# Performance work log

Hardware: AMD Instinct MI355X
Metric: run time of the kernel (lower is better)

## Reference

```python
import jax, jax.numpy as jnp
import numpy as np

N_NODES = 50000
N_EDGES = 800000


def _gcn_conv(x, W, b, src, dst, deg_inv_sqrt, n_nodes):
    # PyG GCNConv: h = x @ W, then symmetric-normalized sum aggregation
    h = x @ W  # [N, F_out]
    norm = deg_inv_sqrt[src] * deg_inv_sqrt[dst]  # [E_aug]
    msg = h[src] * norm[:, None]  # [E_aug, F_out]
    out = jax.ops.segment_sum(msg, dst, num_segments=n_nodes)
    return out + b


def setup_inputs() -> dict:
    key = jax.random.key(0)
    k1, k2, k3, k4 = jax.random.split(key, 4)
    x = jax.random.normal(k1, (N_NODES, 128), dtype=jnp.float32)
    edge_index = jax.random.randint(k2, (2, N_EDGES), 0, N_NODES, dtype=jnp.int64)
    W1 = jax.random.normal(k3, (128, 64), dtype=jnp.float32) * (1.0 / np.sqrt(128))
    b1 = jnp.zeros((64,), dtype=jnp.float32)
    W2 = jax.random.normal(k4, (64, 32), dtype=jnp.float32) * (1.0 / np.sqrt(64))
    b2 = jnp.zeros((32,), dtype=jnp.float32)
    return {"x": x, "edge_index": edge_index, "W1": W1, "b1": b1, "W2": W2, "b2": b2}


def reference(x, edge_index, W1, b1, W2, b2):
    n_nodes = x.shape[0]
    # add self-loops (PyG GCNConv default)
    loop = jnp.arange(n_nodes, dtype=edge_index.dtype)
    src = jnp.concatenate([edge_index[0], loop])
    dst = jnp.concatenate([edge_index[1], loop])
    # symmetric normalization: deg from target index (gcn_norm)
    deg = jax.ops.segment_sum(jnp.ones_like(dst, dtype=x.dtype), dst, num_segments=n_nodes)
    deg_inv_sqrt = jnp.where(deg > 0, jax.lax.rsqrt(jnp.maximum(deg, 1.0)), 0.0)

    h = _gcn_conv(x, W1, b1, src, dst, deg_inv_sqrt, n_nodes)
    h = jax.nn.relu(h)
    # dropout is identity in eval mode (reference runs inference)
    out = _gcn_conv(h, W2, b2, src, dst, deg_inv_sqrt, n_nodes)
    return out
```

## Files before the change

### kernel.cpp

```cpp
#include <hip/hip_runtime.h>
#include <hip/hip_fp16.h>


#define F_IN 128
#define F_MID 64
#define F_OUT 32
#define NBLK 512
#define CAP 8192
#define CAPN 64

#define RFL(x) __builtin_amdgcn_readfirstlane(x)

__device__ __forceinline__ void h8acc(float* a, const uint4& v) {
    const __half2* hp = (const __half2*)&v;
#pragma unroll
    for (int i = 0; i < 4; ++i) {
        float2 f = __half22float2(hp[i]);
        a[2 * i]     += f.x;
        a[2 * i + 1] += f.y;
    }
}

__device__ __forceinline__ void h8unpack(float* f, const uint4& v) {
    const __half2* hp = (const __half2*)&v;
#pragma unroll
    for (int i = 0; i < 4; ++i) {
        float2 t = __half22float2(hp[i]);
        f[2 * i]     = t.x;
        f[2 * i + 1] = t.y;
    }
}

__device__ __forceinline__ uint4 pack8(const float4& a, const float4& b) {
    union { uint4 u; __half2 h[4]; } pk;
    pk.h[0] = __float22half2_rn(make_float2(a.x, a.y));
    pk.h[1] = __float22half2_rn(make_float2(a.z, a.w));
    pk.h[2] = __float22half2_rn(make_float2(b.x, b.y));
    pk.h[3] = __float22half2_rn(make_float2(b.z, b.w));
    return pk.u;
}

__global__ __launch_bounds__(256) void k_build_scatter(
    const int* __restrict__ src, const int* __restrict__ dst, int E, int chunk,
    int nbuk, int* __restrict__ cursor, int* __restrict__ esort) {
    __shared__ int cnt[256];
    __shared__ int off[256];
    int t = threadIdx.x;
    cnt[t] = 0;
    __syncthreads();
    int e0 = blockIdx.x * chunk;
    int e1 = min(E, e0 + chunk);
    for (int e = e0 + t; e < e1; e += 256)
        atomicAdd(&cnt[dst[e] >> 8], 1);
    __syncthreads();
    if (t < nbuk) {
        int c = cnt[t];
        off[t] = t * CAP + (c ? atomicAdd(&cursor[t], c) : 0);
    }
    __syncthreads();
    for (int e = e0 + t; e < e1; e += 256) {
        int d = dst[e];
        int pos = atomicAdd(&off[d >> 8], 1);
        esort[pos] = (src[e] << 8) | (d & 255);
    }
}

__global__ __launch_bounds__(256) void k_bucket_pad(
    const int* __restrict__ esort, const int* __restrict__ cursor, int n,
    int* __restrict__ deg, int* __restrict__ elist) {
    __shared__ int cur[256];
    int b = blockIdx.x;
    int t = threadIdx.x;
    int node0 = b << 8;
    int e0 = b * CAP;
    int e1 = e0 + min(cursor[b], CAP);
    cur[t] = 0;
    __syncthreads();
    for (int e = e0 + t; e < e1; e += 256) {
        int p = esort[e];
        int local = p & 255;
        int pos = atomicAdd(&cur[local], 1);
        if (pos < CAPN)
            elist[((node0 + local) << 6) + pos] = p >> 8;
    }
    __syncthreads();
    int node = node0 + t;
    if (node < n) deg[node] = cur[t];
}

__global__ __launch_bounds__(256, 4) void k_gemm1(
    const float* __restrict__ x, const float* __restrict__ W1,
    const int* __restrict__ deg, uint4* __restrict__ g1h, int n) {
    __shared__ float xs[64 * 129];
    int tid  = threadIdx.x;
    int row0 = blockIdx.x * 64;
    for (int i = tid; i < 64 * (F_IN / 4); i += 256) {
        int r = i >> 5, k4 = i & 31;
        int gr = row0 + r;
        float4 v = make_float4(0.f, 0.f, 0.f, 0.f);
        if (gr < n) v = ((const float4*)x)[(size_t)gr * 32 + k4];
        float* p = &xs[r * 129 + k4 * 4];
        p[0] = v.x; p[1] = v.y; p[2] = v.z; p[3] = v.w;
    }
    __syncthreads();
    int w = RFL(tid >> 6);
    int r = tid & 63;
    const float4* W4 = (const float4*)W1;
    float4 a0 = {0.f,0.f,0.f,0.f}, a1 = a0, a2 = a0, a3 = a0;
#pragma unroll 4
    for (int k = 0; k < F_IN; ++k) {
        float xv = xs[r * 129 + k];
        float4 w0 = W4[k * 16 + w * 4 + 0];
        float4 w1 = W4[k * 16 + w * 4 + 1];
        float4 w2 = W4[k * 16 + w * 4 + 2];
        float4 w3 = W4[k * 16 + w * 4 + 3];
        a0.x += xv * w0.x; a0.y += xv * w0.y; a0.z += xv * w0.z; a0.w += xv * w0.w;
        a1.x += xv * w1.x; a1.y += xv * w1.y; a1.z += xv * w1.z; a1.w += xv * w1.w;
        a2.x += xv * w2.x; a2.y += xv * w2.y; a2.z += xv * w2.z; a2.w += xv * w2.w;
        a3.x += xv * w3.x; a3.y += xv * w3.y; a3.z += xv * w3.z; a3.w += xv * w3.w;
    }
    int gr = row0 + r;
    if (gr < n) {
        float dv = rsqrtf((float)(deg[gr] + 1));
        a0.x *= dv; a0.y *= dv; a0.z *= dv; a0.w *= dv;
        a1.x *= dv; a1.y *= dv; a1.z *= dv; a1.w *= dv;
        a2.x *= dv; a2.y *= dv; a2.z *= dv; a2.w *= dv;
        a3.x *= dv; a3.y *= dv; a3.z *= dv; a3.w *= dv;
        g1h[(size_t)gr * 8 + w * 2 + 0] = pack8(a0, a1);
        g1h[(size_t)gr * 8 + w * 2 + 1] = pack8(a2, a3);
    }
}

__global__ __launch_bounds__(256) void k_gather1(
    const int* __restrict__ deg, const int* __restrict__ elist,
    const uint4* __restrict__ g1h, const float* __restrict__ b1,
    uint4* __restrict__ h16, int n) {
    int wave = RFL(threadIdx.x >> 6);
    int lane = threadIdx.x & 63;
    int q    = lane & 7;
    int slot = lane >> 3;
    int d    = blockIdx.x * 4 + wave;
    if (d >= n) return;
    int rawdeg = RFL(deg[d]);
    int cnt  = min(rawdeg, CAPN);
    int base = d << 6;
    float a[8] = {0,0,0,0,0,0,0,0};
    float b[8] = {0,0,0,0,0,0,0,0};
    if (slot == 0) {
        uint4 v = g1h[(size_t)d * 8 + q];
        h8acc(a, v);
    }
    int j = 0;
    for (; j + 32 <= cnt; j += 32) {
        int s0 = elist[base + j + slot];
        int s1 = elist[base + j + 8 + slot];
        int s2 = elist[base + j + 16 + slot];
        int s3 = elist[base + j + 24 + slot];
        uint4 v0 = g1h[(size_t)s0 * 8 + q];
        uint4 v1 = g1h[(size_t)s1 * 8 + q];
        uint4 v2 = g1h[(size_t)s2 * 8 + q];
        uint4 v3 = g1h[(size_t)s3 * 8 + q];
        h8acc(a, v0); h8acc(b, v1); h8acc(a, v2); h8acc(b, v3);
    }
    for (; j + 16 <= cnt; j += 16) {
        int s0 = elist[base + j + slot];
        int s1 = elist[base + j + 8 + slot];
        uint4 v0 = g1h[(size_t)s0 * 8 + q];
        uint4 v1 = g1h[(size_t)s1 * 8 + q];
        h8acc(a, v0); h8acc(b, v1);
    }
    for (; j + 8 <= cnt; j += 8) {
        int s = elist[base + j + slot];
        uint4 v = g1h[(size_t)s * 8 + q];
        h8acc(a, v);
    }
    if (slot < cnt - j) {
        int s = elist[base + j + slot];
        uint4 v = g1h[(size_t)s * 8 + q];
        h8acc(a, v);
    }
#pragma unroll
    for (int i = 0; i < 8; ++i) a[i] += b[i];
#pragma unroll
    for (int i = 0; i < 8; ++i) a[i] += __shfl_xor(a[i], 8);
#pragma unroll
    for (int i = 0; i < 8; ++i) a[i] += __shfl_xor(a[i], 16);
#pragma unroll
    for (int i = 0; i < 8; ++i) a[i] += __shfl_xor(a[i], 32);
    if (slot == 0) {
        float dv = rsqrtf((float)(rawdeg + 1));
        float4 bv0 = ((const float4*)b1)[q * 2 + 0];
        float4 bv1 = ((const float4*)b1)[q * 2 + 1];
        float4 o0, o1;
        o0.x = fmaxf(a[0] * dv + bv0.x, 0.f);
        o0.y = fmaxf(a[1] * dv + bv0.y, 0.f);
        o0.z = fmaxf(a[2] * dv + bv0.z, 0.f);
        o0.w = fmaxf(a[3] * dv + bv0.w, 0.f);
        o1.x = fmaxf(a[4] * dv + bv1.x, 0.f);
        o1.y = fmaxf(a[5] * dv + bv1.y, 0.f);
        o1.z = fmaxf(a[6] * dv + bv1.z, 0.f);
        o1.w = fmaxf(a[7] * dv + bv1.w, 0.f);
        h16[(size_t)d * 8 + q] = pack8(o0, o1);
    }
}

__global__ __launch_bounds__(256, 4) void k_gemm2(
    const uint4* __restrict__ h16, const float* __restrict__ W2,
    const int* __restrict__ deg, uint4* __restrict__ g2h, int n) {
    __shared__ float hs[64 * 65];
    int tid  = threadIdx.x;
    int row0 = blockIdx.x * 64;
    for (int i = tid; i < 64 * 8; i += 256) {
        int r = i >> 3, q = i & 7;
        int gr = row0 + r;
        float f[8] = {0,0,0,0,0,0,0,0};
        if (gr < n) {
            uint4 v = h16[(size_t)gr * 8 + q];
            h8unpack(f, v);
        }
        float* p = &hs[r * 65 + q * 8];
#pragma unroll
        for (int k = 0; k < 8; ++k) p[k] = f[k];
    }
    __syncthreads();
    int w = RFL(tid >> 6);
    int r = tid & 63;
    const float4* W4 = (const float4*)W2;
    float4 a0 = {0.f,0.f,0.f,0.f}, a1 = a0;
#pragma unroll 4
    for (int k = 0; k < F_MID; ++k) {
        float hv = hs[r * 65 + k];
        float4 w0 = W4[k * 8 + w * 2 + 0];
        float4 w1 = W4[k * 8 + w * 2 + 1];
        a0.x += hv * w0.x; a0.y += hv * w0.y; a0.z += hv * w0.z; a0.w += hv * w0.w;
        a1.x += hv * w1.x; a1.y += hv * w1.y; a1.z += hv * w1.z; a1.w += hv * w1.w;
    }
    int gr = row0 + r;
    if (gr < n) {
        float dv = rsqrtf((float)(deg[gr] + 1));
        a0.x *= dv; a0.y *= dv; a0.z *= dv; a0.w *= dv;
        a1.x *= dv; a1.y *= dv; a1.z *= dv; a1.w *= dv;
        g2h[(size_t)gr * 4 + w] = pack8(a0, a1);
    }
}

__global__ __launch_bounds__(256) void k_gather2(
    const int* __restrict__ deg, const int* __restrict__ elist,
    const uint4* __restrict__ g2h, const float* __restrict__ b2,
    float* __restrict__ out, int n) {
    int wave = RFL(threadIdx.x >> 6);
    int lane = threadIdx.x & 63;
    int q    = lane & 3;
    int slot = lane >> 2;
    int d    = blockIdx.x * 4 + wave;
    if (d >= n) return;
    int rawdeg = RFL(deg[d]);
    int cnt  = min(rawdeg, CAPN);
    int base = d << 6;
    float a[8] = {0,0,0,0,0,0,0,0};
    float b[8] = {0,0,0,0,0,0,0,0};
    if (slot == 0) {
        uint4 v = g2h[(size_t)d * 4 + q];
        h8acc(a, v);
    }
    int j = 0;
    for (; j + 64 <= cnt; j += 64) {
        int s0 = elist[base + j + slot];
        int s1 = elist[base + j + 16 + slot];
        int s2 = elist[base + j + 32 + slot];
        int s3 = elist[base + j + 48 + slot];
        uint4 v0 = g2h[(size_t)s0 * 4 + q];
        uint4 v1 = g2h[(size_t)s1 * 4 + q];
        uint4 v2 = g2h[(size_t)s2 * 4 + q];
        uint4 v3 = g2h[(size_t)s3 * 4 + q];
        h8acc(a, v0); h8acc(b, v1); h8acc(a, v2); h8acc(b, v3);
    }
    for (; j + 32 <= cnt; j += 32) {
        int s0 = elist[base + j + slot];
        int s1 = elist[base + j + 16 + slot];
        uint4 v0 = g2h[(size_t)s0 * 4 + q];
        uint4 v1 = g2h[(size_t)s1 * 4 + q];
        h8acc(a, v0); h8acc(b, v1);
    }
    for (; j + 16 <= cnt; j += 16) {
        int s = elist[base + j + slot];
        uint4 v = g2h[(size_t)s * 4 + q];
        h8acc(a, v);
    }
    if (slot < cnt - j) {
        int s = elist[base + j + slot];
        uint4 v = g2h[(size_t)s * 4 + q];
        h8acc(a, v);
    }
#pragma unroll
    for (int i = 0; i < 8; ++i) a[i] += b[i];
#pragma unroll
    for (int i = 0; i < 8; ++i) a[i] += __shfl_xor(a[i], 4);
#pragma unroll
    for (int i = 0; i < 8; ++i) a[i] += __shfl_xor(a[i], 8);
#pragma unroll
    for (int i = 0; i < 8; ++i) a[i] += __shfl_xor(a[i], 16);
#pragma unroll
    for (int i = 0; i < 8; ++i) a[i] += __shfl_xor(a[i], 32);
    if (slot == 0) {
        float dv = rsqrtf((float)(rawdeg + 1));
        float4 bv0 = ((const float4*)b2)[q * 2 + 0];
        float4 bv1 = ((const float4*)b2)[q * 2 + 1];
        float4 o0, o1;
        o0.x = a[0] * dv + bv0.x;
        o0.y = a[1] * dv + bv0.y;
        o0.z = a[2] * dv + bv0.z;
        o0.w = a[3] * dv + bv0.w;
        o1.x = a[4] * dv + bv1.x;
        o1.y = a[5] * dv + bv1.y;
        o1.z = a[6] * dv + bv1.z;
        o1.w = a[7] * dv + bv1.w;
        float4* O4 = (float4*)out;
        O4[(size_t)d * 8 + q * 2 + 0] = o0;
        O4[(size_t)d * 8 + q * 2 + 1] = o1;
    }
}

extern "C" void kernel_launch(void* const* d_in, const int* in_sizes, int n_in,
                              void* d_out, int out_size, void* d_ws, size_t ws_size,
                              hipStream_t stream) {
    const float* x  = (const float*)d_in[0];
    const int*   ei = (const int*)d_in[1];
    const float* W1 = (const float*)d_in[2];
    const float* b1 = (const float*)d_in[3];
    const float* W2 = (const float*)d_in[4];
    const float* b2 = (const float*)d_in[5];

    int n = in_sizes[0] / F_IN;
    int E = in_sizes[1] / 2;
    const int* src = ei;
    const int* dst = ei + E;

    int nbuk  = (n + 255) >> 8;
    int chunk = (E + NBLK - 1) / NBLK;

    char* ws = (char*)d_ws;
    size_t off = 0;
    auto alloc = [&](size_t bytes) {
        char* p = ws + off;
        off += (bytes + 255) & ~(size_t)255;
        return p;
    };
    int*   cursor = (int*)  alloc((size_t)nbuk * 4);
    int*   esort  = (int*)  alloc((size_t)nbuk * CAP * 4);
    int*   deg    = (int*)  alloc((size_t)n * 4);
    int*   elist  = (int*)  alloc((size_t)n * CAPN * 4);
    uint4* g1h    = (uint4*)alloc((size_t)n * F_MID * 2);
    uint4* h16    = (uint4*)alloc((size_t)n * F_MID * 2);
    uint4* g2h    = (uint4*)alloc((size_t)n * F_OUT * 2);

    hipMemsetAsync(cursor, 0, (size_t)nbuk * 4, stream);
    k_build_scatter<<<NBLK, 256, 0, stream>>>(src, dst, E, chunk, nbuk, cursor, esort);
    k_bucket_pad<<<nbuk, 256, 0, stream>>>(esort, cursor, n, deg, elist);

    k_gemm1<<<(n + 63) / 64, 256, 0, stream>>>(x, W1, deg, g1h, n);
    k_gather1<<<(n + 3) / 4, 256, 0, stream>>>(deg, elist, g1h, b1, h16, n);
    k_gemm2<<<(n + 63) / 64, 256, 0, stream>>>(h16, W2, deg, g2h, n);
    k_gather2<<<(n + 3) / 4, 256, 0, stream>>>(deg, elist, g2h, b2,
                                               (float*)d_out, n);
}
```

Baseline: 173.5 us.

## Merge edge scatter with gemm1 and move degree scaling into bucket pad

The edge bucketing scatter and the first dense GEMM now run as one launch, with separate block ranges handling each, so the GEMM no longer waits on the degree computation. The GEMM writes unscaled fp32 output, and the bucket-pad kernel applies the rsqrt degree scaling and fp16 packing once degrees are known. The fp32 intermediate is aliased with the later h16/g2h buffers. This removes one launch and lets the scatter and GEMM overlap, but adds an extra fp32 write and read of the n×64 intermediate.

Result: no change. 171.0 us (-1.5%).

```diff
diff --git a/kernel.cpp b/kernel.cpp
--- a/kernel.cpp
+++ b/kernel.cpp
@@ -40,34 +40,73 @@
     return pk.u;
 }
 
-__global__ __launch_bounds__(256) void k_build_scatter(
+__global__ __launch_bounds__(256, 4) void k_build_gemm1(
     const int* __restrict__ src, const int* __restrict__ dst, int E, int chunk,
-    int nbuk, int* __restrict__ cursor, int* __restrict__ esort) {
-    __shared__ int cnt[256];
-    __shared__ int off[256];
+    int nbuk, int* __restrict__ cursor, int* __restrict__ esort,
+    const float* __restrict__ x, const float* __restrict__ W1,
+    float* __restrict__ g1raw, int n) {
+    __shared__ float xs[64 * 129];
     int t = threadIdx.x;
-    cnt[t] = 0;
+    if (blockIdx.x < NBLK) {
+        int* cnt = (int*)xs;
+        int* off = ((int*)xs) + 256;
+        cnt[t] = 0;
+        __syncthreads();
+        int e0 = blockIdx.x * chunk;
+        int e1 = min(E, e0 + chunk);
+        for (int e = e0 + t; e < e1; e += 256)
+            atomicAdd(&cnt[dst[e] >> 8], 1);
+        __syncthreads();
+        if (t < nbuk) {
+            int c = cnt[t];
+            off[t] = t * CAP + (c ? atomicAdd(&cursor[t], c) : 0);
+        }
+        __syncthreads();
+        for (int e = e0 + t; e < e1; e += 256) {
+            int d = dst[e];
+            int pos = atomicAdd(&off[d >> 8], 1);
+            esort[pos] = (src[e] << 8) | (d & 255);
+        }
+        return;
+    }
+    int row0 = (blockIdx.x - NBLK) * 64;
+    for (int i = t; i < 64 * (F_IN / 4); i += 256) {
+        int r = i >> 5, k4 = i & 31;
+        int gr = row0 + r;
+        float4 v = make_float4(0.f, 0.f, 0.f, 0.f);
+        if (gr < n) v = ((const float4*)x)[(size_t)gr * 32 + k4];
+        float* p = &xs[r * 129 + k4 * 4];
+        p[0] = v.x; p[1] = v.y; p[2] = v.z; p[3] = v.w;
+    }
     __syncthreads();
-    int e0 = blockIdx.x * chunk;
-    int e1 = min(E, e0 + chunk);
-    for (int e = e0 + t; e < e1; e += 256)
-        atomicAdd(&cnt[dst[e] >> 8], 1);
-    __syncthreads();
-    if (t < nbuk) {
-        int c = cnt[t];
-        off[t] = t * CAP + (c ? atomicAdd(&cursor[t], c) : 0);
-    }
-    __syncthreads();
-    for (int e = e0 + t; e < e1; e += 256) {
-        int d = dst[e];
-        int pos = atomicAdd(&off[d >> 8], 1);
-        esort[pos] = (src[e] << 8) | (d & 255);
-    }
-}
-
-__global__ __launch_bounds__(256) void k_bucket_pad(
+    int w = RFL(t >> 6);
+    int r = t & 63;
+    const float4* W4 = (const float4*)W1;
+    float4 a0 = {0.f,0.f,0.f,0.f}, a1 = a0, a2 = a0, a3 = a0;
+#pragma unroll 4
+    for (int k = 0; k < F_IN; ++k) {
+        float xv = xs[r * 129 + k];
+        float4 w0 = W4[k * 16 + w * 4 + 0];
+        float4 w1 = W4[k * 16 + w * 4 + 1];
+        float4 w2 = W4[k * 16 + w * 4 + 2];
+        float4 w3 = W4[k * 16 + w * 4 + 3];
+        a0.x += xv * w0.x; a0.y += xv * w0.y; a0.z += xv * w0.z; a0.w += xv * w0.w;
+        a1.x += xv * w1.x; a1.y += xv * w1.y; a1.z += xv * w1.z; a1.w += xv * w1.w;
+        a2.x += xv * w2.x; a2.y += xv * w2.y; a2.z += xv * w2.z; a2.w += xv * w2.w;
+        a3.x += xv * w3.x; a3.y += xv * w3.y; a3.z += xv * w3.z; a3.w += xv * w3.w;
+    }
+    int gr = row0 + r;
+    if (gr < n) {
+        float4* G = (float4*)g1raw;
+        size_t base = (size_t)gr * 16 + w * 4;
+        G[base + 0] = a0; G[base + 1] = a1; G[base + 2] = a2; G[base + 3] = a3;
+    }
+}
+
+__global__ __launch_bounds__(256) void k_bucket_pad_scale(
     const int* __restrict__ esort, const int* __restrict__ cursor, int n,
-    int* __restrict__ deg, int* __restrict__ elist) {
+    int* __restrict__ deg, int* __restrict__ elist,
+    const float* __restrict__ g1raw, uint4* __restrict__ g1h) {
     __shared__ int cur[256];
     int b = blockIdx.x;
     int t = threadIdx.x;
@@ -86,48 +125,17 @@
     __syncthreads();
     int node = node0 + t;
     if (node < n) deg[node] = cur[t];
-}
-
-__global__ __launch_bounds__(256, 4) void k_gemm1(
-    const float* __restrict__ x, const float* __restrict__ W1,
-    const int* __restrict__ deg, uint4* __restrict__ g1h, int n) {
-    __shared__ float xs[64 * 129];
-    int tid  = threadIdx.x;
-    int row0 = blockIdx.x * 64;
-    for (int i = tid; i < 64 * (F_IN / 4); i += 256) {
-        int r = i >> 5, k4 = i & 31;
-        int gr = row0 + r;
-        float4 v = make_float4(0.f, 0.f, 0.f, 0.f);
-        if (gr < n) v = ((const float4*)x)[(size_t)gr * 32 + k4];
-        float* p = &xs[r * 129 + k4 * 4];
-        p[0] = v.x; p[1] = v.y; p[2] = v.z; p[3] = v.w;
-    }
-    __syncthreads();
-    int w = RFL(tid >> 6);
-    int r = tid & 63;
-    const float4* W4 = (const float4*)W1;
-    float4 a0 = {0.f,0.f,0.f,0.f}, a1 = a0, a2 = a0, a3 = a0;
-#pragma unroll 4
-    for (int k = 0; k < F_IN; ++k) {
-        float xv = xs[r * 129 + k];
-        float4 w0 = W4[k * 16 + w * 4 + 0];
-        float4 w1 = W4[k * 16 + w * 4 + 1];
-        float4 w2 = W4[k * 16 + w * 4 + 2];
-        float4 w3 = W4[k * 16 + w * 4 + 3];
-        a0.x += xv * w0.x; a0.y += xv * w0.y; a0.z += xv * w0.z; a0.w += xv * w0.w;
-        a1.x += xv * w1.x; a1.y += xv * w1.y; a1.z += xv * w1.z; a1.w += xv * w1.w;
-        a2.x += xv * w2.x; a2.y += xv * w2.y; a2.z += xv * w2.z; a2.w += xv * w2.w;
-        a3.x += xv * w3.x; a3.y += xv * w3.y; a3.z += xv * w3.z; a3.w += xv * w3.w;
-    }
-    int gr = row0 + r;
-    if (gr < n) {
-        float dv = rsqrtf((float)(deg[gr] + 1));
-        a0.x *= dv; a0.y *= dv; a0.z *= dv; a0.w *= dv;
-        a1.x *= dv; a1.y *= dv; a1.z *= dv; a1.w *= dv;
-        a2.x *= dv; a2.y *= dv; a2.z *= dv; a2.w *= dv;
-        a3.x *= dv; a3.y *= dv; a3.z *= dv; a3.w *= dv;
-        g1h[(size_t)gr * 8 + w * 2 + 0] = pack8(a0, a1);
-        g1h[(size_t)gr * 8 + w * 2 + 1] = pack8(a2, a3);
+    for (int i = t; i < 256 * 8; i += 256) {
+        int nl = i >> 3, q = i & 7;
+        int nd = node0 + nl;
+        if (nd < n) {
+            float dv = rsqrtf((float)(cur[nl] + 1));
+            const float4* G = (const float4*)g1raw + (size_t)nd * 16 + q * 2;
+            float4 u = G[0], v = G[1];
+            u.x *= dv; u.y *= dv; u.z *= dv; u.w *= dv;
+            v.x *= dv; v.y *= dv; v.z *= dv; v.w *= dv;
+            g1h[(size_t)nd * 8 + q] = pack8(u, v);
+        }
     }
 }
 
@@ -338,6 +346,7 @@
 
     int nbuk  = (n + 255) >> 8;
     int chunk = (E + NBLK - 1) / NBLK;
+    int ngemm = (n + 63) / 64;
 
     char* ws = (char*)d_ws;
     size_t off = 0;
@@ -351,14 +360,20 @@
     int*   deg    = (int*)  alloc((size_t)n * 4);
     int*   elist  = (int*)  alloc((size_t)n * CAPN * 4);
     uint4* g1h    = (uint4*)alloc((size_t)n * F_MID * 2);
-    uint4* h16    = (uint4*)alloc((size_t)n * F_MID * 2);
-    uint4* g2h    = (uint4*)alloc((size_t)n * F_OUT * 2);
+    size_t raw_bytes = (size_t)n * F_MID * 4;
+    size_t hb        = (size_t)n * F_MID * 2;
+    size_t g2b       = (size_t)n * F_OUT * 2;
+    char*  region = alloc(raw_bytes > hb + g2b ? raw_bytes : hb + g2b);
+    float* g1raw  = (float*)region;
+    uint4* h16    = (uint4*)region;
+    uint4* g2h    = (uint4*)(region + hb);
 
     hipMemsetAsync(cursor, 0, (size_t)nbuk * 4, stream);
-    k_build_scatter<<<NBLK, 256, 0, stream>>>(src, dst, E, chunk, nbuk, cursor, esort);
-    k_bucket_pad<<<nbuk, 256, 0, stream>>>(esort, cursor, n, deg, elist);
-
-    k_gemm1<<<(n + 63) / 64, 256, 0, stream>>>(x, W1, deg, g1h, n);
+    k_build_gemm1<<<NBLK + ngemm, 256, 0, stream>>>(
+        src, dst, E, chunk, nbuk, cursor, esort, x, W1, g1raw, n);
+    k_bucket_pad_scale<<<nbuk, 256, 0, stream>>>(
+        esort, cursor, n, deg, elist, g1raw, g1h);
+
     k_gather1<<<(n + 3) / 4, 256, 0, stream>>>(deg, elist, g1h, b1, h16, n);
     k_gemm2<<<(n + 63) / 64, 256, 0, stream>>>(h16, W2, deg, g2h, n);
     k_gather2<<<(n + 3) / 4, 256, 0, stream>>>(deg, elist, g2h, b2,
```
